# Kernel tuning notes

Measured on AMD Instinct MI355X. Metric: run time of the kernel, lower is better.

## Reference

```python
import jax, jax.numpy as jnp
import numpy as np

EPS_W = 1e-9


def area2d(a, b, c):
    # signed parallelogram area; a/b/c are [..., >=2] points
    return (b[..., 0] - a[..., 0]) * (c[..., 1] - a[..., 1]) - (b[..., 1] - a[..., 1]) * (c[..., 0] - a[..., 0])


def lookup_table(size):
    # square table of 2d points (x, y) in [-1, 1], matching torch meshgrid('ij') + rot90
    lin = jnp.linspace(-1.0, 1.0, size, dtype=jnp.float32)
    xx, yy = jnp.meshgrid(lin, lin, indexing='ij')
    t = jnp.stack([xx, yy], axis=-1)
    return jnp.rot90(t, 1, axes=(0, 1))  # [S,S,2]


def grid_sample_bilinear(img, grid):
    # img [C,H,W]; grid [...,2] with (x,y) in [-1,1]; bilinear, zero padding, align_corners=True
    C, H, W = img.shape
    x, y = grid[..., 0], grid[..., 1]
    ix = (x + 1.0) * (W - 1) * 0.5
    iy = (y + 1.0) * (H - 1) * 0.5
    ix0 = jnp.floor(ix)
    iy0 = jnp.floor(iy)
    ix1 = ix0 + 1.0
    iy1 = iy0 + 1.0
    wx1 = ix - ix0
    wx0 = 1.0 - wx1
    wy1 = iy - iy0
    wy0 = 1.0 - wy1

    def tap(iyf, ixf):
        inb = (ixf >= 0) & (ixf <= W - 1) & (iyf >= 0) & (iyf <= H - 1)
        ii = jnp.clip(ixf, 0, W - 1).astype(jnp.int32)
        jj = jnp.clip(iyf, 0, H - 1).astype(jnp.int32)
        return img[:, jj, ii] * inb.astype(img.dtype)  # [C, ...]

    return (tap(iy0, ix0) * (wy0 * wx0) + tap(iy0, ix1) * (wy0 * wx1)
            + tap(iy1, ix0) * (wy1 * wx0) + tap(iy1, ix1) * (wy1 * wx1))


def _render(vertices, uv, uvmap, faces, uvfaces, size):
    pts = lookup_table(size)              # [S,S,2]
    uvn = uv * 2.0 - 1.0                  # uv scaled to [-1,1] as in __init__
    tris = vertices[faces]                # [K,3,3]
    uvt = uvn[uvfaces]                    # [K,3,2]

    # backface cull mask (z-component of cross(v1-v0, v2-v0) > 0)
    e1 = tris[:, 1] - tris[:, 0]
    e2 = tris[:, 2] - tris[:, 0]
    normal_z = e1[:, 0] * e2[:, 1] - e1[:, 1] * e2[:, 0]
    valid = normal_z > 0

    zinit = jnp.min(vertices, axis=0)[-1]
    result0 = jnp.zeros((4, size, size), jnp.float32)
    zbuf0 = jnp.full((size, size), zinit, dtype=jnp.float32)

    def step(carry, xs):
        result, zbuf = carry
        tri, uvtri, ok = xs               # tri [3,3], uvtri [3,2], ok scalar bool
        tri2d = tri[:, :2]
        w = area2d(tri2d[0], tri2d[1], tri2d[2])
        # sub areas against every pixel (dense equivalent of AABB + inside masks)
        pAB = area2d(tri2d[1], pts, tri2d[0])   # [S,S]
        pCB = area2d(tri2d[2], pts, tri2d[1])
        pCA = area2d(tri2d[0], pts, tri2d[2])
        inside = (pAB > 0) & (pCB > 0) & (pCA > 0)
        ws = jnp.where(w >= EPS_W, w, 1.0)      # safe divide; masked out below
        w1 = pCB / ws
        w2 = pCA / ws
        w3 = 1.0 - w1 - w2
        z = w1 * tri[0, 2] + w2 * tri[1, 2] + w3 * tri[2, 2]   # [S,S]
        mask = ok & (w >= EPS_W) & inside & (z >= zbuf)
        # barycentric uv interpolation + bilinear texture lookup
        ptsUV = w1[..., None] * uvtri[0] + w2[..., None] * uvtri[1] + w3[..., None] * uvtri[2]  # [S,S,2]
        rgb = grid_sample_bilinear(uvmap, ptsUV)  # [3,S,S]
        zbuf = jnp.where(mask, z, zbuf)
        rgba = jnp.concatenate([rgb, jnp.ones((1, size, size), result.dtype)], axis=0)
        result = jnp.where(mask[None], rgba, result)
        return (result, zbuf), None

    (result, _), _ = jax.lax.scan(step, (result0, zbuf0), (tris, uvt, valid))
    return result


def setup_inputs() -> dict:
    key = jax.random.key(0)
    k0, k1, k2, k3, k4 = jax.random.split(key, 5)
    V, K, M, T, S = 1500, 1500, 2000, 1024, 512
    vertices = jax.random.normal(k0, (V, 3), dtype=jnp.float32)
    faces = jax.random.randint(k1, (K, 3), 0, V)
    uv = jax.random.uniform(k2, (M, 2), dtype=jnp.float32)
    uvfaces = jax.random.randint(k3, (K, 3), 0, M)
    uvmap = jax.random.normal(k4, (3, T, T), dtype=jnp.float32)
    return {"vertices": vertices, "faces": faces, "uv": uv,
            "uvfaces": uvfaces, "uvmap": uvmap, "size": S}


def reference(vertices, faces, uv, uvfaces, uvmap, size):
    return _render(vertices, uv, uvmap, faces, uvfaces, size)
```

## Files before the change

### kernel.cpp

```cpp
#include <hip/hip_runtime.h>
#include <hip/hip_fp16.h>
#include <cmath>

#pragma clang fp contract(off)

#define MAXK 2048

struct TriUV {
  float u0x, u0y, u1x, u1y;
  float u2x, u2y, pad0, pad1;
};

__device__ __forceinline__ float h2f(unsigned v) {
  __half_raw r; r.x = (unsigned short)v;
  return __half2float(__half(r));
}
__device__ __forceinline__ unsigned f2h(float v) {
  return (unsigned)__half_as_ushort(__float2half(v));
}
__device__ __forceinline__ unsigned pkh(float lo, float hi) {
  return f2h(lo) | (f2h(hi) << 16);
}
__device__ __forceinline__ unsigned fmapu(float f) {
  unsigned b = __float_as_uint(f);
  return (b & 0x80000000u) ? ~b : (b | 0x80000000u);
}
__device__ __forceinline__ float funmap(unsigned m) {
  return __uint_as_float((m & 0x80000000u) ? (m ^ 0x80000000u) : ~m);
}

__device__ __forceinline__ float lin_at(int i, int n) {
#pragma clang fp contract(off)
  if (i == n - 1) return 1.0f;
  float step = (float)i / (float)(n - 1);
  return (-1.0f) * (1.0f - step) + 1.0f * step;
}

__global__ __launch_bounds__(256) void prep_kernel(
    const float* __restrict__ verts, const int* __restrict__ faces,
    const float* __restrict__ uv, const int* __restrict__ uvfaces, int V, int K,
    float4* __restrict__ q0S, float4* __restrict__ q1S,
    float4* __restrict__ q2S, float4* __restrict__ q3S,
    float4* __restrict__ bboxS, uint4* __restrict__ apS,
    float4* __restrict__ metaS, float4* __restrict__ planeS,
    TriUV* __restrict__ tuv, float* __restrict__ zinit) {
#pragma clang fp contract(off)
  __shared__ float smz[256];
  int tid = (int)threadIdx.x;
  int bid = (int)blockIdx.x;
  if (bid == 0) {
    float m = 3.402823466e38f;
    for (int i = tid; i < V; i += 256) m = fminf(m, verts[3 * i + 2]);
    smz[tid] = m;
    __syncthreads();
    for (int s2 = 128; s2 > 0; s2 >>= 1) {
      if (tid < s2) smz[tid] = fminf(smz[tid], smz[tid + s2]);
      __syncthreads();
    }
    if (tid == 0) *zinit = smz[0];
    return;
  }
  int t = (bid - 1) * 256 + tid;
  if (t >= K) return;
  int i0 = faces[3 * t + 0], i1 = faces[3 * t + 1], i2 = faces[3 * t + 2];
  float t0x = verts[3 * i0 + 0], t0y = verts[3 * i0 + 1], z0 = verts[3 * i0 + 2];
  float t1x = verts[3 * i1 + 0], t1y = verts[3 * i1 + 1], z1 = verts[3 * i1 + 2];
  float t2x = verts[3 * i2 + 0], t2y = verts[3 * i2 + 1], z2 = verts[3 * i2 + 2];
  int j0 = uvfaces[3 * t + 0], j1 = uvfaces[3 * t + 1], j2 = uvfaces[3 * t + 2];
  TriUV u;
  u.u0x = uv[2 * j0 + 0] * 2.0f - 1.0f;
  u.u0y = uv[2 * j0 + 1] * 2.0f - 1.0f;
  u.u1x = uv[2 * j1 + 0] * 2.0f - 1.0f;
  u.u1y = uv[2 * j1 + 1] * 2.0f - 1.0f;
  u.u2x = uv[2 * j2 + 0] * 2.0f - 1.0f;
  u.u2y = uv[2 * j2 + 1] * 2.0f - 1.0f;
  u.pad0 = 0.0f; u.pad1 = 0.0f;
  tuv[t] = u;
  float w = (t1x - t0x) * (t2y - t0y) - (t1y - t0y) * (t2x - t0x);
  if (w < 1e-9f) {
    bboxS[t] = make_float4(3.0e38f, -3.0e38f, 3.0e38f, -3.0e38f);
    return;
  }
  float dAy = t0y - t1y, dAx = t0x - t1x;
  float dBy = t1y - t2y, dBx = t1x - t2x;
  float dCy = t2y - t0y, dCx = t2x - t0x;
  q0S[t] = make_float4(t1x, t1y, dAy, dAx);
  q1S[t] = make_float4(t2x, t2y, dBy, dBx);
  q2S[t] = make_float4(t0x, t0y, dCy, dCx);
  q3S[t] = make_float4(z0, z1, z2, w);
  bboxS[t] = make_float4(fminf(fminf(t0x, t1x), t2x),
                         fmaxf(fmaxf(t0x, t1x), t2x),
                         fminf(fminf(t0y, t1y), t2y),
                         fmaxf(fmaxf(t0y, t1y), t2y));
  float fA = t1y * dAx - t1x * dAy;
  float fB = t2y * dBx - t2x * dBy;
  float fC = t0y * dCx - t0x * dCy;
  float sA = fabsf(dAy) + fabsf(dAx) + fabsf(fA);
  float sB = fabsf(dBy) + fabsf(dBx) + fabsf(fB);
  float sC = fabsf(dCy) + fabsf(dCx) + fabsf(fC);
  float M = fmaxf(fmaxf(sA, sB), sC) * 9.766e-4f + 1e-4f;
  apS[t] = make_uint4(pkh(dAy, dAx), pkh(fA, dBy), pkh(dBx, fB),
                      pkh(dCy, dCx));
  metaS[t] = make_float4(M, fC, __int_as_float(t), 0.0f);
  float zmx = fmaxf(fmaxf(z0, z1), z2);
  float gatef = zmx + 1e-3f + 1e-4f / w;
  float gx = (z0 * dBy + z1 * dCy + z2 * dAy) / w;
  float gy = -(z0 * dBx + z1 * dCx + z2 * dAx) / w;
  float cc = (z0 * fB + z1 * fC + z2 * fA) / w;
  float mm = (fabsf(z0 * fB) + fabsf(z1 * fC) + fabsf(z2 * fA) +
              fabsf(z0 * dBy) + fabsf(z1 * dCy) + fabsf(z2 * dAy) +
              fabsf(z0 * dBx) + fabsf(z1 * dCx) + fabsf(z2 * dAx)) *
                 (2e-6f / w) +
             1e-3f + 1e-4f / w + 1e-4f;
  planeS[t] = make_float4(gx, gy, cc + mm, gatef);
}

__global__ __launch_bounds__(1024) void render_kernel(
    const float4* __restrict__ q0S, const float4* __restrict__ q1S,
    const float4* __restrict__ q2S, const float4* __restrict__ q3S,
    const float4* __restrict__ bboxS, const uint4* __restrict__ apS,
    const float4* __restrict__ metaS, const float4* __restrict__ planeS,
    int N, const TriUV* __restrict__ tuv, const float* __restrict__ zinitp,
    const float* __restrict__ uvmap, int T, float* __restrict__ out, int S) {
#pragma clang fp contract(off)
  __shared__ unsigned short s_kept[MAXK];
  __shared__ unsigned s_tgm[MAXK];
  __shared__ unsigned s_em[MAXK];
  __shared__ unsigned long long s_key[256];
  __shared__ unsigned s_zu[256];
  __shared__ unsigned s_hist[256];
  __shared__ int s_cur[256];
  __shared__ unsigned s_wsum[4];

  int tid = (int)threadIdx.x;
  int wv = tid >> 6, ln = tid & 63;
  int s = wv >> 2, q = wv & 3;
  int pix = (q << 6) + ln;
  int tilesX = S >> 4;
  int tileX = (int)blockIdx.x % tilesX;
  int tileY = (int)blockIdx.x / tilesX;
  int j = (tileX << 4) + (pix & 15);
  int i = (tileY << 4) + (pix >> 4);
  float px = lin_at(j, S);
  float py = lin_at(S - 1 - i, S);
  float pxlo = lin_at(tileX << 4, S);
  float pxhi = lin_at((tileX << 4) + 15, S);
  float pylo = lin_at(S - 1 - ((tileY << 4) + 15), S);
  float pyhi = lin_at(S - 1 - (tileY << 4), S);

  float zinit = *zinitp;
  unsigned zinit_m = fmapu(zinit);
  if (tid < 256) {
    s_zu[tid] = zinit_m;
    s_key[tid] = ((unsigned long long)zinit_m << 32);
    s_hist[tid] = 0u;
  }
  volatile unsigned* vzu = s_zu;
  __syncthreads();

  bool kA = false, kB = false;
  int bA = 0, bB = 0;
  unsigned gA = 0, gB = 0;
  {
    int t = tid;
    if (t < N) {
      float4 bb = bboxS[t];
      if (bb.x <= pxhi && bb.y >= pxlo && bb.z <= pyhi && bb.w >= pylo) {
        float4 pl = planeS[t];
        float ub = pl.z + fmaxf(pl.x * pxlo, pl.x * pxhi) +
                   fmaxf(pl.y * pylo, pl.y * pyhi);
        float tg = fminf(pl.w, ub);
        kA = true;
        bA = min(max((int)((4.0f - tg) * 32.0f), 0), 255);
        gA = fmapu(tg);
      }
    }
    t = tid + 1024;
    if (t < N) {
      float4 bb = bboxS[t];
      if (bb.x <= pxhi && bb.y >= pxlo && bb.z <= pyhi && bb.w >= pylo) {
        float4 pl = planeS[t];
        float ub = pl.z + fmaxf(pl.x * pxlo, pl.x * pxhi) +
                   fmaxf(pl.y * pylo, pl.y * pyhi);
        float tg = fminf(pl.w, ub);
        kB = true;
        bB = min(max((int)((4.0f - tg) * 32.0f), 0), 255);
        gB = fmapu(tg);
      }
    }
  }
  if (kA) atomicAdd(&s_hist[bA], 1u);
  if (kB) atomicAdd(&s_hist[bB], 1u);
  __syncthreads();
  unsigned hx = 0, hinc = 0;
  if (tid < 256) {
    hx = s_hist[tid];
    unsigned v = hx;
#pragma unroll
    for (int d = 1; d < 64; d <<= 1) {
      unsigned tv = __shfl_up(v, d, 64);
      if (ln >= d) v += tv;
    }
    if (ln == 63) s_wsum[wv] = v;
    hinc = v;
  }
  __syncthreads();
  if (tid < 256) {
    unsigned add = 0;
    for (int w2 = 0; w2 < wv; ++w2) add += s_wsum[w2];
    hinc += add;
    s_hist[tid] = hinc;
    s_cur[tid] = (int)(hinc - hx);
  }
  __syncthreads();
  int nk = (int)s_hist[255];
  if (kA) {
    int sl = atomicAdd(&s_cur[bA], 1);
    s_kept[sl] = (unsigned short)tid;
    s_tgm[sl] = gA;
    float ef = (bA == 0) ? 3.402823466e38f : (4.0f - (float)bA * 0.03125f);
    s_em[sl] = fmapu(ef);
  }
  if (kB) {
    int sl = atomicAdd(&s_cur[bB], 1);
    s_kept[sl] = (unsigned short)(tid + 1024);
    s_tgm[sl] = gB;
    float ef = (bB == 0) ? 3.402823466e38f : (4.0f - (float)bB * 0.03125f);
    s_em[sl] = fmapu(ef);
  }
  __syncthreads();

  for (int a = s; a < nk; a += 4) {
    unsigned em = s_em[a];
    unsigned zb = vzu[pix];
    if (__all(em < zb)) break;
    if (em >= zb && s_tgm[a] >= zb) {
      int idx = s_kept[a];
      uint4 ap = apS[idx];
      float4 mt = metaS[idx];
      float M = mt.x, fC = mt.y;
      float aA = fmaf(px, h2f(ap.x & 0xffffu),
                      fmaf(-py, h2f(ap.x >> 16), h2f(ap.y & 0xffffu)));
      float aB = fmaf(px, h2f(ap.y >> 16),
                      fmaf(-py, h2f(ap.z & 0xffffu), h2f(ap.z >> 16)));
      float aC = fmaf(px, h2f(ap.w & 0xffffu),
                      fmaf(-py, h2f(ap.w >> 16), fC));
      if (fminf(fminf(aA, aB), aC) > -M) {
        float4 q0 = q0S[idx], q1 = q1S[idx], q2 = q2S[idx];
        float pAB = (px - q0.x) * q0.z - (py - q0.y) * q0.w;
        float pCB = (px - q1.x) * q1.z - (py - q1.y) * q1.w;
        float pCA = (px - q2.x) * q2.z - (py - q2.y) * q2.w;
        if (pAB > 0.0f && pCB > 0.0f && pCA > 0.0f) {
          float4 q3 = q3S[idx];
          float w = q3.w;
          float bzf = funmap(vzu[pix]);
          float zs = (pCB * q3.x + pCA * q3.y) + ((w - pCB) - pCA) * q3.z;
          if (w < 1e-3f || zs >= (bzf - 1e-3f) * w) {
            float w1 = pCB / w;
            float w2 = pCA / w;
            float w3 = (1.0f - w1) - w2;
            float z = (w1 * q3.x + w2 * q3.y) + w3 * q3.z;
            int o = __float_as_int(mt.z);
            unsigned zm = fmapu(z);
            unsigned long long key =
                ((unsigned long long)zm << 32) | (unsigned)(o + 1);
            atomicMax(&s_key[pix], key);
            atomicMax(&s_zu[pix], zm);
          }
        }
      }
    }
  }
  __syncthreads();

  if (tid < 256) {
    unsigned long long key = s_key[tid];
    unsigned oP1 = (unsigned)(key & 0xFFFFFFFFULL);
    float o0 = 0.0f, o1 = 0.0f, o2 = 0.0f, o3 = 0.0f;
    if (oP1 != 0) {
      int o = (int)oP1 - 1;
      float4 q1 = q1S[o], q2 = q2S[o], q3 = q3S[o];
      float pCB = (px - q1.x) * q1.z - (py - q1.y) * q1.w;
      float pCA = (px - q2.x) * q2.z - (py - q2.y) * q2.w;
      float w1 = pCB / q3.w;
      float w2 = pCA / q3.w;
      float w3 = (1.0f - w1) - w2;
      TriUV u = tuv[o];
      float x = (w1 * u.u0x + w2 * u.u1x) + w3 * u.u2x;
      float y = (w1 * u.u0y + w2 * u.u1y) + w3 * u.u2y;
      float WH = (float)(T - 1);
      float fx = ((x + 1.0f) * WH) * 0.5f;
      float fy = ((y + 1.0f) * WH) * 0.5f;
      float ix0 = floorf(fx), iy0 = floorf(fy);
      float ix1 = ix0 + 1.0f, iy1 = iy0 + 1.0f;
      float wx1 = fx - ix0, wx0 = 1.0f - wx1;
      float wy1 = fy - iy0, wy0 = 1.0f - wy1;
      float w00 = wy0 * wx0, w01 = wy0 * wx1;
      float w10 = wy1 * wx0, w11 = wy1 * wx1;
      bool bx0 = (ix0 >= 0.0f) && (ix0 <= WH);
      bool bx1 = (ix1 >= 0.0f) && (ix1 <= WH);
      bool by0 = (iy0 >= 0.0f) && (iy0 <= WH);
      bool by1 = (iy1 >= 0.0f) && (iy1 <= WH);
      float m00 = (by0 && bx0) ? 1.0f : 0.0f;
      float m01 = (by0 && bx1) ? 1.0f : 0.0f;
      float m10 = (by1 && bx0) ? 1.0f : 0.0f;
      float m11 = (by1 && bx1) ? 1.0f : 0.0f;
      int cx0 = (int)fminf(fmaxf(ix0, 0.0f), WH);
      int cx1 = (int)fminf(fmaxf(ix1, 0.0f), WH);
      int cy0 = (int)fminf(fmaxf(iy0, 0.0f), WH);
      int cy1 = (int)fminf(fmaxf(iy1, 0.0f), WH);
      int TT = T * T;
      int i00 = cy0 * T + cx0, i01 = cy0 * T + cx1;
      int i10 = cy1 * T + cx0, i11 = cy1 * T + cx1;
      {
        const float* img = uvmap;
        float v00 = img[i00] * m00, v01 = img[i01] * m01;
        float v10 = img[i10] * m10, v11 = img[i11] * m11;
        o0 = ((v00 * w00 + v01 * w01) + v10 * w10) + v11 * w11;
      }
      {
        const float* img = uvmap + TT;
        float v00 = img[i00] * m00, v01 = img[i01] * m01;
        float v10 = img[i10] * m10, v11 = img[i11] * m11;
        o1 = ((v00 * w00 + v01 * w01) + v10 * w10) + v11 * w11;
      }
      {
        const float* img = uvmap + 2 * TT;
        float v00 = img[i00] * m00, v01 = img[i01] * m01;
        float v10 = img[i10] * m10, v11 = img[i11] * m11;
        o2 = ((v00 * w00 + v01 * w01) + v10 * w10) + v11 * w11;
      }
      o3 = 1.0f;
    }
    int p = i * S + j;
    int SS = S * S;
    out[p] = o0;
    out[SS + p] = o1;
    out[2 * SS + p] = o2;
    out[3 * SS + p] = o3;
  }
}

extern "C" void kernel_launch(void* const* d_in, const int* in_sizes, int n_in,
                              void* d_out, int out_size, void* d_ws,
                              size_t ws_size, hipStream_t stream) {
  const float* verts = (const float*)d_in[0];
  const int* faces = (const int*)d_in[1];
  const float* uv = (const float*)d_in[2];
  const int* uvfaces = (const int*)d_in[3];
  const float* uvmap = (const float*)d_in[4];
  int V = in_sizes[0] / 3;
  int K = in_sizes[1] / 3;
  int T = (int)lroundf(sqrtf((float)(in_sizes[4] / 3)));
  int S = (int)lroundf(sqrtf((float)(out_size / 4)));
  float* outp = (float*)d_out;

  char* ws = (char*)d_ws;
  size_t off = 0;
  auto alloc = [&](size_t bytes) {
    void* p = ws + off;
    off = (off + bytes + 255) & ~(size_t)255;
    return p;
  };
  float* zinit = (float*)alloc(4);
  float4* q0S = (float4*)alloc((size_t)MAXK * 16);
  float4* q1S = (float4*)alloc((size_t)MAXK * 16);
  float4* q2S = (float4*)alloc((size_t)MAXK * 16);
  float4* q3S = (float4*)alloc((size_t)MAXK * 16);
  float4* bboxS = (float4*)alloc((size_t)MAXK * 16);
  uint4* apS = (uint4*)alloc((size_t)MAXK * 16);
  float4* metaS = (float4*)alloc((size_t)MAXK * 16);
  float4* planeS = (float4*)alloc((size_t)MAXK * 16);
  TriUV* tuv = (TriUV*)alloc((size_t)K * sizeof(TriUV));

  int pblocks = 1 + (K + 255) / 256;
  prep_kernel<<<pblocks, 256, 0, stream>>>(verts, faces, uv, uvfaces, V, K,
                                           q0S, q1S, q2S, q3S, bboxS, apS,
                                           metaS, planeS, tuv, zinit);
  int tiles = (S >> 4) * (S >> 4);
  render_kernel<<<tiles, 1024, 0, stream>>>(q0S, q1S, q2S, q3S, bboxS, apS,
                                            metaS, planeS, K, tuv, zinit,
                                            uvmap, T, outp, S);
}
```

Before: 32.57 us.

## Batch triangle culling per wavefront with ballot and strided shared layout

Stores the per-triangle conservative depth arrays in a slice-interleaved layout so each of the four wave slices reads a contiguous range. Each wave then loads 64 candidate triangles at once, takes the wave-wide minimum of the current depth buffer, and uses a ballot to iterate only over triangles that could pass the depth test, with the triangle index made wave-uniform. This replaces the per-triangle serial loop, where every lane checked every triangle, and is meant to cut shared-memory loads and divergent work. It adds a shuffle reduction per chunk and serial iteration over the ballot bits, and the early exit now triggers per 64-triangle chunk.

```diff
diff --git a/kernel.cpp b/kernel.cpp
--- a/kernel.cpp
+++ b/kernel.cpp
@@ -217,58 +217,83 @@
   if (kA) {
     int sl = atomicAdd(&s_cur[bA], 1);
     s_kept[sl] = (unsigned short)tid;
-    s_tgm[sl] = gA;
+    int g = (sl & 3) * 512 + (sl >> 2);
+    s_tgm[g] = gA;
     float ef = (bA == 0) ? 3.402823466e38f : (4.0f - (float)bA * 0.03125f);
-    s_em[sl] = fmapu(ef);
+    s_em[g] = fmapu(ef);
   }
   if (kB) {
     int sl = atomicAdd(&s_cur[bB], 1);
     s_kept[sl] = (unsigned short)(tid + 1024);
-    s_tgm[sl] = gB;
+    int g = (sl & 3) * 512 + (sl >> 2);
+    s_tgm[g] = gB;
     float ef = (bB == 0) ? 3.402823466e38f : (4.0f - (float)bB * 0.03125f);
-    s_em[sl] = fmapu(ef);
-  }
-  __syncthreads();
-
-  for (int a = s; a < nk; a += 4) {
-    unsigned em = s_em[a];
-    unsigned zb = vzu[pix];
-    if (__all(em < zb)) break;
-    if (em >= zb && s_tgm[a] >= zb) {
-      int idx = s_kept[a];
-      uint4 ap = apS[idx];
-      float4 mt = metaS[idx];
-      float M = mt.x, fC = mt.y;
-      float aA = fmaf(px, h2f(ap.x & 0xffffu),
-                      fmaf(-py, h2f(ap.x >> 16), h2f(ap.y & 0xffffu)));
-      float aB = fmaf(px, h2f(ap.y >> 16),
-                      fmaf(-py, h2f(ap.z & 0xffffu), h2f(ap.z >> 16)));
-      float aC = fmaf(px, h2f(ap.w & 0xffffu),
-                      fmaf(-py, h2f(ap.w >> 16), fC));
-      if (fminf(fminf(aA, aB), aC) > -M) {
-        float4 q0 = q0S[idx], q1 = q1S[idx], q2 = q2S[idx];
-        float pAB = (px - q0.x) * q0.z - (py - q0.y) * q0.w;
-        float pCB = (px - q1.x) * q1.z - (py - q1.y) * q1.w;
-        float pCA = (px - q2.x) * q2.z - (py - q2.y) * q2.w;
-        if (pAB > 0.0f && pCB > 0.0f && pCA > 0.0f) {
-          float4 q3 = q3S[idx];
-          float w = q3.w;
-          float bzf = funmap(vzu[pix]);
-          float zs = (pCB * q3.x + pCA * q3.y) + ((w - pCB) - pCA) * q3.z;
-          if (w < 1e-3f || zs >= (bzf - 1e-3f) * w) {
-            float w1 = pCB / w;
-            float w2 = pCA / w;
-            float w3 = (1.0f - w1) - w2;
-            float z = (w1 * q3.x + w2 * q3.y) + w3 * q3.z;
-            int o = __float_as_int(mt.z);
-            unsigned zm = fmapu(z);
-            unsigned long long key =
-                ((unsigned long long)zm << 32) | (unsigned)(o + 1);
-            atomicMax(&s_key[pix], key);
-            atomicMax(&s_zu[pix], zm);
+    s_em[g] = fmapu(ef);
+  }
+  __syncthreads();
+
+  {
+    int ecount = (nk > s) ? ((nk - 1 - s) >> 2) + 1 : 0;
+    const unsigned* tg_s = s_tgm + (s << 9);
+    const unsigned* em_s = s_em + (s << 9);
+    for (int cb = 0; cb < ecount; cb += 64) {
+      int e = cb + ln;
+      bool val = e < ecount;
+      unsigned tg = val ? tg_s[e] : 0u;
+      unsigned emv = val ? em_s[e] : 0u;
+      unsigned zbl = vzu[pix];
+      unsigned zbmin = zbl;
+#pragma unroll
+      for (int m2 = 1; m2 < 64; m2 <<= 1) {
+        unsigned o2 = (unsigned)__shfl_xor((int)zbmin, m2, 64);
+        zbmin = min(zbmin, o2);
+      }
+      unsigned long long cand = __ballot(val && tg >= zbmin);
+      while (cand) {
+        int k = (int)(__ffsll((long long)cand) - 1);
+        cand &= cand - 1;
+        unsigned tgm_k = (unsigned)__shfl((int)tg, k, 64);
+        unsigned zbn = vzu[pix];
+        if (tgm_k >= zbn) {
+          int a = ((cb + k) << 2) + s;
+          int idx = (int)s_kept[a];
+          idx = __builtin_amdgcn_readfirstlane(idx);
+          uint4 ap = apS[idx];
+          float4 mt = metaS[idx];
+          float M = mt.x, fC = mt.y;
+          float aA = fmaf(px, h2f(ap.x & 0xffffu),
+                          fmaf(-py, h2f(ap.x >> 16), h2f(ap.y & 0xffffu)));
+          float aB = fmaf(px, h2f(ap.y >> 16),
+                          fmaf(-py, h2f(ap.z & 0xffffu), h2f(ap.z >> 16)));
+          float aC = fmaf(px, h2f(ap.w & 0xffffu),
+                          fmaf(-py, h2f(ap.w >> 16), fC));
+          if (fminf(fminf(aA, aB), aC) > -M) {
+            float4 q0 = q0S[idx], q1 = q1S[idx], q2 = q2S[idx];
+            float pAB = (px - q0.x) * q0.z - (py - q0.y) * q0.w;
+            float pCB = (px - q1.x) * q1.z - (py - q1.y) * q1.w;
+            float pCA = (px - q2.x) * q2.z - (py - q2.y) * q2.w;
+            if (pAB > 0.0f && pCB > 0.0f && pCA > 0.0f) {
+              float4 q3 = q3S[idx];
+              float w = q3.w;
+              float bzf = funmap(vzu[pix]);
+              float zs = (pCB * q3.x + pCA * q3.y) + ((w - pCB) - pCA) * q3.z;
+              if (w < 1e-3f || zs >= (bzf - 1e-3f) * w) {
+                float w1 = pCB / w;
+                float w2 = pCA / w;
+                float w3 = (1.0f - w1) - w2;
+                float z = (w1 * q3.x + w2 * q3.y) + w3 * q3.z;
+                int o = __float_as_int(mt.z);
+                unsigned zm = fmapu(z);
+                unsigned long long key =
+                    ((unsigned long long)zm << 32) | (unsigned)(o + 1);
+                atomicMax(&s_key[pix], key);
+                atomicMax(&s_zu[pix], zm);
+              }
+            }
           }
         }
       }
+      if (__all((int)(!val || emv < zbmin))) break;
     }
   }
   __syncthreads();
```

Result: slower. 44.51 us (+36.6%).

## Software-pipeline the per-triangle loop and pack gate values into uint2

Applied to the files above, without the earlier changes.

Restructures the main candidate-triangle loop so the next iteration's gate values, triangle index and global ap/meta records are loaded ahead of use, which is meant to hide global-memory latency behind the current triangle's tests. The two shared gate arrays are merged into one uint2 array so each iteration needs a single shared load. Tile Y assignment is skewed by tileX, apparently to spread heavy tiles across blocks. The skew is a pure permutation of tiles, so correctness is preserved. In exchange the loop uses more registers. It also reads the depth buffer one iteration early for the early-exit check, and the per-pixel em>=zb test is dropped, so some extra triangles may be tested.

```diff
diff --git a/kernel.cpp b/kernel.cpp
--- a/kernel.cpp
+++ b/kernel.cpp
@@ -124,8 +124,7 @@
     const float* __restrict__ uvmap, int T, float* __restrict__ out, int S) {
 #pragma clang fp contract(off)
   __shared__ unsigned short s_kept[MAXK];
-  __shared__ unsigned s_tgm[MAXK];
-  __shared__ unsigned s_em[MAXK];
+  __shared__ uint2 s_gates[MAXK];
   __shared__ unsigned long long s_key[256];
   __shared__ unsigned s_zu[256];
   __shared__ unsigned s_hist[256];
@@ -137,8 +136,10 @@
   int s = wv >> 2, q = wv & 3;
   int pix = (q << 6) + ln;
   int tilesX = S >> 4;
-  int tileX = (int)blockIdx.x % tilesX;
-  int tileY = (int)blockIdx.x / tilesX;
+  int tilesY = S >> 4;
+  int b = (int)blockIdx.x;
+  int tileX = b % tilesX;
+  int tileY = (b / tilesX + tileX) % tilesY;
   int j = (tileX << 4) + (pix & 15);
   int i = (tileY << 4) + (pix >> 4);
   float px = lin_at(j, S);
@@ -217,58 +218,72 @@
   if (kA) {
     int sl = atomicAdd(&s_cur[bA], 1);
     s_kept[sl] = (unsigned short)tid;
-    s_tgm[sl] = gA;
     float ef = (bA == 0) ? 3.402823466e38f : (4.0f - (float)bA * 0.03125f);
-    s_em[sl] = fmapu(ef);
+    s_gates[sl] = make_uint2(fmapu(ef), gA);
   }
   if (kB) {
     int sl = atomicAdd(&s_cur[bB], 1);
     s_kept[sl] = (unsigned short)(tid + 1024);
-    s_tgm[sl] = gB;
     float ef = (bB == 0) ? 3.402823466e38f : (4.0f - (float)bB * 0.03125f);
-    s_em[sl] = fmapu(ef);
-  }
-  __syncthreads();
-
-  for (int a = s; a < nk; a += 4) {
-    unsigned em = s_em[a];
+    s_gates[sl] = make_uint2(fmapu(ef), gB);
+  }
+  __syncthreads();
+
+  if (nk > s) {
+    int aN = s + 4;  if (aN >= nk) aN = s;
+    uint2 g0 = s_gates[s];
+    uint2 g1 = s_gates[aN];
+    int i0 = (int)s_kept[s];
+    int i1 = (int)s_kept[aN];
+    uint4 ap0 = apS[i0];
+    float4 mt0 = metaS[i0];
     unsigned zb = vzu[pix];
-    if (__all(em < zb)) break;
-    if (em >= zb && s_tgm[a] >= zb) {
-      int idx = s_kept[a];
-      uint4 ap = apS[idx];
-      float4 mt = metaS[idx];
-      float M = mt.x, fC = mt.y;
-      float aA = fmaf(px, h2f(ap.x & 0xffffu),
-                      fmaf(-py, h2f(ap.x >> 16), h2f(ap.y & 0xffffu)));
-      float aB = fmaf(px, h2f(ap.y >> 16),
-                      fmaf(-py, h2f(ap.z & 0xffffu), h2f(ap.z >> 16)));
-      float aC = fmaf(px, h2f(ap.w & 0xffffu),
-                      fmaf(-py, h2f(ap.w >> 16), fC));
-      if (fminf(fminf(aA, aB), aC) > -M) {
-        float4 q0 = q0S[idx], q1 = q1S[idx], q2 = q2S[idx];
-        float pAB = (px - q0.x) * q0.z - (py - q0.y) * q0.w;
-        float pCB = (px - q1.x) * q1.z - (py - q1.y) * q1.w;
-        float pCA = (px - q2.x) * q2.z - (py - q2.y) * q2.w;
-        if (pAB > 0.0f && pCB > 0.0f && pCA > 0.0f) {
-          float4 q3 = q3S[idx];
-          float w = q3.w;
-          float bzf = funmap(vzu[pix]);
-          float zs = (pCB * q3.x + pCA * q3.y) + ((w - pCB) - pCA) * q3.z;
-          if (w < 1e-3f || zs >= (bzf - 1e-3f) * w) {
-            float w1 = pCB / w;
-            float w2 = pCA / w;
-            float w3 = (1.0f - w1) - w2;
-            float z = (w1 * q3.x + w2 * q3.y) + w3 * q3.z;
-            int o = __float_as_int(mt.z);
-            unsigned zm = fmapu(z);
-            unsigned long long key =
-                ((unsigned long long)zm << 32) | (unsigned)(o + 1);
-            atomicMax(&s_key[pix], key);
-            atomicMax(&s_zu[pix], zm);
+    for (int a = s; a < nk; a += 4) {
+      unsigned em = g0.x, tg = g0.y;
+      int an2 = a + 8;  if (an2 >= nk) an2 = a;
+      uint2 g2 = s_gates[an2];
+      int i2 = (int)s_kept[an2];
+      uint4 ap1 = apS[i1];
+      float4 mt1 = metaS[i1];
+      unsigned zbn = vzu[pix];
+      if (__all(em < zb)) break;
+      if (tg >= zb) {
+        float M = mt0.x, fC = mt0.y;
+        float aA = fmaf(px, h2f(ap0.x & 0xffffu),
+                        fmaf(-py, h2f(ap0.x >> 16), h2f(ap0.y & 0xffffu)));
+        float aB = fmaf(px, h2f(ap0.y >> 16),
+                        fmaf(-py, h2f(ap0.z & 0xffffu), h2f(ap0.z >> 16)));
+        float aC = fmaf(px, h2f(ap0.w & 0xffffu),
+                        fmaf(-py, h2f(ap0.w >> 16), fC));
+        if (fminf(fminf(aA, aB), aC) > -M) {
+          float4 q0 = q0S[i0], q1 = q1S[i0], q2 = q2S[i0];
+          float pAB = (px - q0.x) * q0.z - (py - q0.y) * q0.w;
+          float pCB = (px - q1.x) * q1.z - (py - q1.y) * q1.w;
+          float pCA = (px - q2.x) * q2.z - (py - q2.y) * q2.w;
+          if (pAB > 0.0f && pCB > 0.0f && pCA > 0.0f) {
+            float4 q3 = q3S[i0];
+            float w = q3.w;
+            float bzf = funmap(vzu[pix]);
+            float zs = (pCB * q3.x + pCA * q3.y) + ((w - pCB) - pCA) * q3.z;
+            if (w < 1e-3f || zs >= (bzf - 1e-3f) * w) {
+              float w1 = pCB / w;
+              float w2 = pCA / w;
+              float w3 = (1.0f - w1) - w2;
+              float z = (w1 * q3.x + w2 * q3.y) + w3 * q3.z;
+              int o = __float_as_int(mt0.z);
+              unsigned zm = fmapu(z);
+              unsigned long long key =
+                  ((unsigned long long)zm << 32) | (unsigned)(o + 1);
+              atomicMax(&s_key[pix], key);
+              atomicMax(&s_zu[pix], zm);
+            }
           }
         }
       }
+      g0 = g1; g1 = g2;
+      i0 = i1; i1 = i2;
+      ap0 = ap1; mt0 = mt1;
+      zb = zbn;
     }
   }
   __syncthreads();
```

Result: slower. 33.95 us (+4.2%).

## Use persistent render blocks with atomic tile queue and packed gate pairs

Applied to the files above, without the earlier changes.

The render kernel now launches at most 512 persistent blocks that repeatedly pull 16x16 tiles from a global atomic counter, which prep_kernel resets. The goal is to balance the uneven per-tile work and cut the cost of launching and retiring 1024 blocks. The two per-triangle gate arrays are packed into one uint2 shared array so a single LDS load serves both, and the redundant em>=zb check is dropped. In exchange, each tile adds a global atomic and extra barriers. It also re-initialises shared state every tile and serialises tiles within each block.

```diff
diff --git a/kernel.cpp b/kernel.cpp
--- a/kernel.cpp
+++ b/kernel.cpp
@@ -43,12 +43,14 @@
     float4* __restrict__ q2S, float4* __restrict__ q3S,
     float4* __restrict__ bboxS, uint4* __restrict__ apS,
     float4* __restrict__ metaS, float4* __restrict__ planeS,
-    TriUV* __restrict__ tuv, float* __restrict__ zinit) {
+    TriUV* __restrict__ tuv, float* __restrict__ zinit,
+    int* __restrict__ tileCtr) {
 #pragma clang fp contract(off)
   __shared__ float smz[256];
   int tid = (int)threadIdx.x;
   int bid = (int)blockIdx.x;
   if (bid == 0) {
+    if (tid == 0) *tileCtr = 0;
     float m = 3.402823466e38f;
     for (int i = tid; i < V; i += 256) m = fminf(m, verts[3 * i + 2]);
     smz[tid] = m;
@@ -121,223 +123,233 @@
     const float4* __restrict__ bboxS, const uint4* __restrict__ apS,
     const float4* __restrict__ metaS, const float4* __restrict__ planeS,
     int N, const TriUV* __restrict__ tuv, const float* __restrict__ zinitp,
-    const float* __restrict__ uvmap, int T, float* __restrict__ out, int S) {
+    const float* __restrict__ uvmap, int T, float* __restrict__ out, int S,
+    int* __restrict__ tileCtr) {
 #pragma clang fp contract(off)
   __shared__ unsigned short s_kept[MAXK];
-  __shared__ unsigned s_tgm[MAXK];
-  __shared__ unsigned s_em[MAXK];
+  __shared__ uint2 s_gates[MAXK];
   __shared__ unsigned long long s_key[256];
   __shared__ unsigned s_zu[256];
   __shared__ unsigned s_hist[256];
   __shared__ int s_cur[256];
   __shared__ unsigned s_wsum[4];
+  __shared__ int s_tile;
 
   int tid = (int)threadIdx.x;
   int wv = tid >> 6, ln = tid & 63;
   int s = wv >> 2, q = wv & 3;
   int pix = (q << 6) + ln;
   int tilesX = S >> 4;
-  int tileX = (int)blockIdx.x % tilesX;
-  int tileY = (int)blockIdx.x / tilesX;
-  int j = (tileX << 4) + (pix & 15);
-  int i = (tileY << 4) + (pix >> 4);
-  float px = lin_at(j, S);
-  float py = lin_at(S - 1 - i, S);
-  float pxlo = lin_at(tileX << 4, S);
-  float pxhi = lin_at((tileX << 4) + 15, S);
-  float pylo = lin_at(S - 1 - ((tileY << 4) + 15), S);
-  float pyhi = lin_at(S - 1 - (tileY << 4), S);
-
+  int tilesTotal = tilesX * (S >> 4);
   float zinit = *zinitp;
   unsigned zinit_m = fmapu(zinit);
-  if (tid < 256) {
-    s_zu[tid] = zinit_m;
-    s_key[tid] = ((unsigned long long)zinit_m << 32);
-    s_hist[tid] = 0u;
-  }
   volatile unsigned* vzu = s_zu;
-  __syncthreads();
-
-  bool kA = false, kB = false;
-  int bA = 0, bB = 0;
-  unsigned gA = 0, gB = 0;
-  {
-    int t = tid;
-    if (t < N) {
-      float4 bb = bboxS[t];
-      if (bb.x <= pxhi && bb.y >= pxlo && bb.z <= pyhi && bb.w >= pylo) {
-        float4 pl = planeS[t];
-        float ub = pl.z + fmaxf(pl.x * pxlo, pl.x * pxhi) +
-                   fmaxf(pl.y * pylo, pl.y * pyhi);
-        float tg = fminf(pl.w, ub);
-        kA = true;
-        bA = min(max((int)((4.0f - tg) * 32.0f), 0), 255);
-        gA = fmapu(tg);
-      }
-    }
-    t = tid + 1024;
-    if (t < N) {
-      float4 bb = bboxS[t];
-      if (bb.x <= pxhi && bb.y >= pxlo && bb.z <= pyhi && bb.w >= pylo) {
-        float4 pl = planeS[t];
-        float ub = pl.z + fmaxf(pl.x * pxlo, pl.x * pxhi) +
-                   fmaxf(pl.y * pylo, pl.y * pyhi);
-        float tg = fminf(pl.w, ub);
-        kB = true;
-        bB = min(max((int)((4.0f - tg) * 32.0f), 0), 255);
-        gB = fmapu(tg);
-      }
-    }
-  }
-  if (kA) atomicAdd(&s_hist[bA], 1u);
-  if (kB) atomicAdd(&s_hist[bB], 1u);
-  __syncthreads();
-  unsigned hx = 0, hinc = 0;
-  if (tid < 256) {
-    hx = s_hist[tid];
-    unsigned v = hx;
+
+  for (;;) {
+    if (tid == 0) s_tile = atomicAdd(tileCtr, 1);
+    __syncthreads();
+    int tile = s_tile;
+    if (tile >= tilesTotal) break;
+
+    int tileX = tile % tilesX;
+    int tileY = tile / tilesX;
+    int j = (tileX << 4) + (pix & 15);
+    int i = (tileY << 4) + (pix >> 4);
+    float px = lin_at(j, S);
+    float py = lin_at(S - 1 - i, S);
+    float pxlo = lin_at(tileX << 4, S);
+    float pxhi = lin_at((tileX << 4) + 15, S);
+    float pylo = lin_at(S - 1 - ((tileY << 4) + 15), S);
+    float pyhi = lin_at(S - 1 - (tileY << 4), S);
+
+    if (tid < 256) {
+      s_zu[tid] = zinit_m;
+      s_key[tid] = ((unsigned long long)zinit_m << 32);
+      s_hist[tid] = 0u;
+    }
+    __syncthreads();
+
+    bool kA = false, kB = false;
+    int bA = 0, bB = 0;
+    unsigned gA = 0, gB = 0;
+    {
+      int t = tid;
+      if (t < N) {
+        float4 bb = bboxS[t];
+        if (bb.x <= pxhi && bb.y >= pxlo && bb.z <= pyhi && bb.w >= pylo) {
+          float4 pl = planeS[t];
+          float ub = pl.z + fmaxf(pl.x * pxlo, pl.x * pxhi) +
+                     fmaxf(pl.y * pylo, pl.y * pyhi);
+          float tg = fminf(pl.w, ub);
+          kA = true;
+          bA = min(max((int)((4.0f - tg) * 32.0f), 0), 255);
+          gA = fmapu(tg);
+        }
+      }
+      t = tid + 1024;
+      if (t < N) {
+        float4 bb = bboxS[t];
+        if (bb.x <= pxhi && bb.y >= pxlo && bb.z <= pyhi && bb.w >= pylo) {
+          float4 pl = planeS[t];
+          float ub = pl.z + fmaxf(pl.x * pxlo, pl.x * pxhi) +
+                     fmaxf(pl.y * pylo, pl.y * pyhi);
+          float tg = fminf(pl.w, ub);
+          kB = true;
+          bB = min(max((int)((4.0f - tg) * 32.0f), 0), 255);
+          gB = fmapu(tg);
+        }
+      }
+    }
+    if (kA) atomicAdd(&s_hist[bA], 1u);
+    if (kB) atomicAdd(&s_hist[bB], 1u);
+    __syncthreads();
+    unsigned hx = 0, hinc = 0;
+    if (tid < 256) {
+      hx = s_hist[tid];
+      unsigned v = hx;
 #pragma unroll
-    for (int d = 1; d < 64; d <<= 1) {
-      unsigned tv = __shfl_up(v, d, 64);
-      if (ln >= d) v += tv;
-    }
-    if (ln == 63) s_wsum[wv] = v;
-    hinc = v;
-  }
-  __syncthreads();
-  if (tid < 256) {
-    unsigned add = 0;
-    for (int w2 = 0; w2 < wv; ++w2) add += s_wsum[w2];
-    hinc += add;
-    s_hist[tid] = hinc;
-    s_cur[tid] = (int)(hinc - hx);
-  }
-  __syncthreads();
-  int nk = (int)s_hist[255];
-  if (kA) {
-    int sl = atomicAdd(&s_cur[bA], 1);
-    s_kept[sl] = (unsigned short)tid;
-    s_tgm[sl] = gA;
-    float ef = (bA == 0) ? 3.402823466e38f : (4.0f - (float)bA * 0.03125f);
-    s_em[sl] = fmapu(ef);
-  }
-  if (kB) {
-    int sl = atomicAdd(&s_cur[bB], 1);
-    s_kept[sl] = (unsigned short)(tid + 1024);
-    s_tgm[sl] = gB;
-    float ef = (bB == 0) ? 3.402823466e38f : (4.0f - (float)bB * 0.03125f);
-    s_em[sl] = fmapu(ef);
-  }
-  __syncthreads();
-
-  for (int a = s; a < nk; a += 4) {
-    unsigned em = s_em[a];
-    unsigned zb = vzu[pix];
-    if (__all(em < zb)) break;
-    if (em >= zb && s_tgm[a] >= zb) {
-      int idx = s_kept[a];
-      uint4 ap = apS[idx];
-      float4 mt = metaS[idx];
-      float M = mt.x, fC = mt.y;
-      float aA = fmaf(px, h2f(ap.x & 0xffffu),
-                      fmaf(-py, h2f(ap.x >> 16), h2f(ap.y & 0xffffu)));
-      float aB = fmaf(px, h2f(ap.y >> 16),
-                      fmaf(-py, h2f(ap.z & 0xffffu), h2f(ap.z >> 16)));
-      float aC = fmaf(px, h2f(ap.w & 0xffffu),
-                      fmaf(-py, h2f(ap.w >> 16), fC));
-      if (fminf(fminf(aA, aB), aC) > -M) {
-        float4 q0 = q0S[idx], q1 = q1S[idx], q2 = q2S[idx];
-        float pAB = (px - q0.x) * q0.z - (py - q0.y) * q0.w;
+      for (int d = 1; d < 64; d <<= 1) {
+        unsigned tv = __shfl_up(v, d, 64);
+        if (ln >= d) v += tv;
+      }
+      if (ln == 63) s_wsum[wv] = v;
+      hinc = v;
+    }
+    __syncthreads();
+    if (tid < 256) {
+      unsigned add = 0;
+      for (int w2 = 0; w2 < wv; ++w2) add += s_wsum[w2];
+      hinc += add;
+      s_hist[tid] = hinc;
+      s_cur[tid] = (int)(hinc - hx);
+    }
+    __syncthreads();
+    int nk = (int)s_hist[255];
+    if (kA) {
+      int sl = atomicAdd(&s_cur[bA], 1);
+      s_kept[sl] = (unsigned short)tid;
+      float ef = (bA == 0) ? 3.402823466e38f : (4.0f - (float)bA * 0.03125f);
+      s_gates[sl] = make_uint2(fmapu(ef), gA);
+    }
+    if (kB) {
+      int sl = atomicAdd(&s_cur[bB], 1);
+      s_kept[sl] = (unsigned short)(tid + 1024);
+      float ef = (bB == 0) ? 3.402823466e38f : (4.0f - (float)bB * 0.03125f);
+      s_gates[sl] = make_uint2(fmapu(ef), gB);
+    }
+    __syncthreads();
+
+    for (int a = s; a < nk; a += 4) {
+      uint2 g = s_gates[a];
+      unsigned em = g.x;
+      unsigned zb = vzu[pix];
+      if (__all(em < zb)) break;
+      if (g.y >= zb) {
+        int idx = (int)s_kept[a];
+        uint4 ap = apS[idx];
+        float4 mt = metaS[idx];
+        float M = mt.x, fC = mt.y;
+        float aA = fmaf(px, h2f(ap.x & 0xffffu),
+                        fmaf(-py, h2f(ap.x >> 16), h2f(ap.y & 0xffffu)));
+        float aB = fmaf(px, h2f(ap.y >> 16),
+                        fmaf(-py, h2f(ap.z & 0xffffu), h2f(ap.z >> 16)));
+        float aC = fmaf(px, h2f(ap.w & 0xffffu),
+                        fmaf(-py, h2f(ap.w >> 16), fC));
+        if (fminf(fminf(aA, aB), aC) > -M) {
+          float4 q0 = q0S[idx], q1 = q1S[idx], q2 = q2S[idx];
+          float pAB = (px - q0.x) * q0.z - (py - q0.y) * q0.w;
+          float pCB = (px - q1.x) * q1.z - (py - q1.y) * q1.w;
+          float pCA = (px - q2.x) * q2.z - (py - q2.y) * q2.w;
+          if (pAB > 0.0f && pCB > 0.0f && pCA > 0.0f) {
+            float4 q3 = q3S[idx];
+            float w = q3.w;
+            float bzf = funmap(vzu[pix]);
+            float zs = (pCB * q3.x + pCA * q3.y) + ((w - pCB) - pCA) * q3.z;
+            if (w < 1e-3f || zs >= (bzf - 1e-3f) * w) {
+              float w1 = pCB / w;
+              float w2 = pCA / w;
+              float w3 = (1.0f - w1) - w2;
+              float z = (w1 * q3.x + w2 * q3.y) + w3 * q3.z;
+              int o = __float_as_int(mt.z);
+              unsigned zm = fmapu(z);
+              unsigned long long key =
+                  ((unsigned long long)zm << 32) | (unsigned)(o + 1);
+              atomicMax(&s_key[pix], key);
+              atomicMax(&s_zu[pix], zm);
+            }
+          }
+        }
+      }
+    }
+    __syncthreads();
+
+    if (tid < 256) {
+      unsigned long long key = s_key[tid];
+      unsigned oP1 = (unsigned)(key & 0xFFFFFFFFULL);
+      float o0 = 0.0f, o1 = 0.0f, o2 = 0.0f, o3 = 0.0f;
+      if (oP1 != 0) {
+        int o = (int)oP1 - 1;
+        float4 q1 = q1S[o], q2 = q2S[o], q3 = q3S[o];
         float pCB = (px - q1.x) * q1.z - (py - q1.y) * q1.w;
         float pCA = (px - q2.x) * q2.z - (py - q2.y) * q2.w;
-        if (pAB > 0.0f && pCB > 0.0f && pCA > 0.0f) {
-          float4 q3 = q3S[idx];
-          float w = q3.w;
-          float bzf = funmap(vzu[pix]);
-          float zs = (pCB * q3.x + pCA * q3.y) + ((w - pCB) - pCA) * q3.z;
-          if (w < 1e-3f || zs >= (bzf - 1e-3f) * w) {
-            float w1 = pCB / w;
-            float w2 = pCA / w;
-            float w3 = (1.0f - w1) - w2;
-            float z = (w1 * q3.x + w2 * q3.y) + w3 * q3.z;
-            int o = __float_as_int(mt.z);
-            unsigned zm = fmapu(z);
-            unsigned long long key =
-                ((unsigned long long)zm << 32) | (unsigned)(o + 1);
-            atomicMax(&s_key[pix], key);
-            atomicMax(&s_zu[pix], zm);
-          }
-        }
-      }
-    }
-  }
-  __syncthreads();
-
-  if (tid < 256) {
-    unsigned long long key = s_key[tid];
-    unsigned oP1 = (unsigned)(key & 0xFFFFFFFFULL);
-    float o0 = 0.0f, o1 = 0.0f, o2 = 0.0f, o3 = 0.0f;
-    if (oP1 != 0) {
-      int o = (int)oP1 - 1;
-      float4 q1 = q1S[o], q2 = q2S[o], q3 = q3S[o];
-      float pCB = (px - q1.x) * q1.z - (py - q1.y) * q1.w;
-      float pCA = (px - q2.x) * q2.z - (py - q2.y) * q2.w;
-      float w1 = pCB / q3.w;
-      float w2 = pCA / q3.w;
-      float w3 = (1.0f - w1) - w2;
-      TriUV u = tuv[o];
-      float x = (w1 * u.u0x + w2 * u.u1x) + w3 * u.u2x;
-      float y = (w1 * u.u0y + w2 * u.u1y) + w3 * u.u2y;
-      float WH = (float)(T - 1);
-      float fx = ((x + 1.0f) * WH) * 0.5f;
-      float fy = ((y + 1.0f) * WH) * 0.5f;
-      float ix0 = floorf(fx), iy0 = floorf(fy);
-      float ix1 = ix0 + 1.0f, iy1 = iy0 + 1.0f;
-      float wx1 = fx - ix0, wx0 = 1.0f - wx1;
-      float wy1 = fy - iy0, wy0 = 1.0f - wy1;
-      float w00 = wy0 * wx0, w01 = wy0 * wx1;
-      float w10 = wy1 * wx0, w11 = wy1 * wx1;
-      bool bx0 = (ix0 >= 0.0f) && (ix0 <= WH);
-      bool bx1 = (ix1 >= 0.0f) && (ix1 <= WH);
-      bool by0 = (iy0 >= 0.0f) && (iy0 <= WH);
-      bool by1 = (iy1 >= 0.0f) && (iy1 <= WH);
-      float m00 = (by0 && bx0) ? 1.0f : 0.0f;
-      float m01 = (by0 && bx1) ? 1.0f : 0.0f;
-      float m10 = (by1 && bx0) ? 1.0f : 0.0f;
-      float m11 = (by1 && bx1) ? 1.0f : 0.0f;
-      int cx0 = (int)fminf(fmaxf(ix0, 0.0f), WH);
-      int cx1 = (int)fminf(fmaxf(ix1, 0.0f), WH);
-      int cy0 = (int)fminf(fmaxf(iy0, 0.0f), WH);
-      int cy1 = (int)fminf(fmaxf(iy1, 0.0f), WH);
-      int TT = T * T;
-      int i00 = cy0 * T + cx0, i01 = cy0 * T + cx1;
-      int i10 = cy1 * T + cx0, i11 = cy1 * T + cx1;
-      {
-        const float* img = uvmap;
-        float v00 = img[i00] * m00, v01 = img[i01] * m01;
-        float v10 = img[i10] * m10, v11 = img[i11] * m11;
-        o0 = ((v00 * w00 + v01 * w01) + v10 * w10) + v11 * w11;
-      }
-      {
-        const float* img = uvmap + TT;
-        float v00 = img[i00] * m00, v01 = img[i01] * m01;
-        float v10 = img[i10] * m10, v11 = img[i11] * m11;
-        o1 = ((v00 * w00 + v01 * w01) + v10 * w10) + v11 * w11;
-      }
-      {
-        const float* img = uvmap + 2 * TT;
-        float v00 = img[i00] * m00, v01 = img[i01] * m01;
-        float v10 = img[i10] * m10, v11 = img[i11] * m11;
-        o2 = ((v00 * w00 + v01 * w01) + v10 * w10) + v11 * w11;
-      }
-      o3 = 1.0f;
-    }
-    int p = i * S + j;
-    int SS = S * S;
-    out[p] = o0;
-    out[SS + p] = o1;
-    out[2 * SS + p] = o2;
-    out[3 * SS + p] = o3;
+        float w1 = pCB / q3.w;
+        float w2 = pCA / q3.w;
+        float w3 = (1.0f - w1) - w2;
+        TriUV u = tuv[o];
+        float x = (w1 * u.u0x + w2 * u.u1x) + w3 * u.u2x;
+        float y = (w1 * u.u0y + w2 * u.u1y) + w3 * u.u2y;
+        float WH = (float)(T - 1);
+        float fx = ((x + 1.0f) * WH) * 0.5f;
+        float fy = ((y + 1.0f) * WH) * 0.5f;
+        float ix0 = floorf(fx), iy0 = floorf(fy);
+        float ix1 = ix0 + 1.0f, iy1 = iy0 + 1.0f;
+        float wx1 = fx - ix0, wx0 = 1.0f - wx1;
+        float wy1 = fy - iy0, wy0 = 1.0f - wy1;
+        float w00 = wy0 * wx0, w01 = wy0 * wx1;
+        float w10 = wy1 * wx0, w11 = wy1 * wx1;
+        bool bx0 = (ix0 >= 0.0f) && (ix0 <= WH);
+        bool bx1 = (ix1 >= 0.0f) && (ix1 <= WH);
+        bool by0 = (iy0 >= 0.0f) && (iy0 <= WH);
+        bool by1 = (iy1 >= 0.0f) && (iy1 <= WH);
+        float m00 = (by0 && bx0) ? 1.0f : 0.0f;
+        float m01 = (by0 && bx1) ? 1.0f : 0.0f;
+        float m10 = (by1 && bx0) ? 1.0f : 0.0f;
+        float m11 = (by1 && bx1) ? 1.0f : 0.0f;
+        int cx0 = (int)fminf(fmaxf(ix0, 0.0f), WH);
+        int cx1 = (int)fminf(fmaxf(ix1, 0.0f), WH);
+        int cy0 = (int)fminf(fmaxf(iy0, 0.0f), WH);
+        int cy1 = (int)fminf(fmaxf(iy1, 0.0f), WH);
+        int TT = T * T;
+        int i00 = cy0 * T + cx0, i01 = cy0 * T + cx1;
+        int i10 = cy1 * T + cx0, i11 = cy1 * T + cx1;
+        {
+          const float* img = uvmap;
+          float v00 = img[i00] * m00, v01 = img[i01] * m01;
+          float v10 = img[i10] * m10, v11 = img[i11] * m11;
+          o0 = ((v00 * w00 + v01 * w01) + v10 * w10) + v11 * w11;
+        }
+        {
+          const float* img = uvmap + TT;
+          float v00 = img[i00] * m00, v01 = img[i01] * m01;
+          float v10 = img[i10] * m10, v11 = img[i11] * m11;
+          o1 = ((v00 * w00 + v01 * w01) + v10 * w10) + v11 * w11;
+        }
+        {
+          const float* img = uvmap + 2 * TT;
+          float v00 = img[i00] * m00, v01 = img[i01] * m01;
+          float v10 = img[i10] * m10, v11 = img[i11] * m11;
+          o2 = ((v00 * w00 + v01 * w01) + v10 * w10) + v11 * w11;
+        }
+        o3 = 1.0f;
+      }
+      int p = i * S + j;
+      int SS = S * S;
+      out[p] = o0;
+      out[SS + p] = o1;
+      out[2 * SS + p] = o2;
+      out[3 * SS + p] = o3;
+    }
+    __syncthreads();
   }
 }
 
@@ -363,6 +375,7 @@
     return p;
   };
   float* zinit = (float*)alloc(4);
+  int* tileCtr = (int*)alloc(4);
   float4* q0S = (float4*)alloc((size_t)MAXK * 16);
   float4* q1S = (float4*)alloc((size_t)MAXK * 16);
   float4* q2S = (float4*)alloc((size_t)MAXK * 16);
@@ -376,9 +389,10 @@
   int pblocks = 1 + (K + 255) / 256;
   prep_kernel<<<pblocks, 256, 0, stream>>>(verts, faces, uv, uvfaces, V, K,
                                            q0S, q1S, q2S, q3S, bboxS, apS,
-                                           metaS, planeS, tuv, zinit);
+                                           metaS, planeS, tuv, zinit, tileCtr);
   int tiles = (S >> 4) * (S >> 4);
-  render_kernel<<<tiles, 1024, 0, stream>>>(q0S, q1S, q2S, q3S, bboxS, apS,
-                                            metaS, planeS, K, tuv, zinit,
-                                            uvmap, T, outp, S);
-}
+  int rblocks = tiles < 512 ? tiles : 512;
+  render_kernel<<<rblocks, 1024, 0, stream>>>(q0S, q1S, q2S, q3S, bboxS, apS,
+                                              metaS, planeS, K, tuv, zinit,
+                                              uvmap, T, outp, S, tileCtr);
+}
```

New measurement: 43.08 us. 32.3% more time.
